# Kernel optimization log

Measured on AMD Instinct MI355X. Metric: run time of the kernel, lower is better.

## Reference

```python
import jax, jax.numpy as jnp
import numpy as np

B, N, H, S = 128, 20, 128, 2   # batch, num_nodes (= sequence_size), hidden, static feats
STEPS = 5 * N                  # max_steps in the torch loop; mask=depot=ones never breaks


def setup_inputs() -> dict:
    key = jax.random.key(0)
    ks = jax.random.split(key, 16)
    rn = lambda k, shape, s=0.1: jax.random.normal(k, shape, dtype=jnp.float32) * s
    z = lambda shape: jnp.zeros(shape, jnp.float32)
    return {
        "adj": jax.random.uniform(ks[0], (B, N, N), dtype=jnp.float32),
        "static": jax.random.uniform(ks[1], (B, S, N), dtype=jnp.float32),
        "dynamic": jax.random.uniform(ks[2], (B, S, N), dtype=jnp.float32),
        "depot": jnp.ones((B, N), jnp.float32),   # mask; log(1)=0 so never masks out
        # 1x1 Conv1d encoders == per-node linear maps (H, C_in)
        "W_adj": rn(ks[3], (H, N + 1)), "b_adj": z((H,)),
        "W_stat": rn(ks[4], (H, S)), "b_stat": z((H,)),
        "W_dyn": rn(ks[5], (H, S)), "b_dyn": z((H,)),
        "W_dec": rn(ks[6], (H, S)), "b_dec": z((H,)),
        # GRU (1 layer), torch gate order: r, z, n
        "gru_Wih": rn(ks[7], (3 * H, H)), "gru_Whh": rn(ks[8], (3 * H, H)),
        "gru_bih": z((3 * H,)), "gru_bhh": z((3 * H,)),
        # Attention: v (H,), W (H, 4H) over concat(adj_h, static_h, dyn_h, rnn)
        "attn_v": rn(ks[9], (H,)), "attn_W": rn(ks[10], (H, 4 * H)),
        # Pointer head: v (H,), W (H, 2H) over concat(static_h, context)
        "ptr_v": rn(ks[11], (H,)), "ptr_W": rn(ks[12], (H, 2 * H)),
        "x0": z((S,)),  # initial decoder input (torch: zeros)
    }


def reference(adj, static, dynamic, depot,
              W_adj, b_adj, W_stat, b_stat, W_dyn, b_dyn, W_dec, b_dec,
              gru_Wih, gru_Whh, gru_bih, gru_bhh,
              attn_v, attn_W, ptr_v, ptr_W, x0):
    # encode once (1x1 convs)
    adj_in = jnp.concatenate([adj, depot[:, None, :]], axis=1)      # (B, N+1, N)
    adj_h = jnp.einsum('hc,bcn->bhn', W_adj, adj_in) + b_adj[None, :, None]
    stat_h = jnp.einsum('hc,bcn->bhn', W_stat, static) + b_stat[None, :, None]
    dyn_h = jnp.einsum('hc,bcn->bhn', W_dyn, dynamic) + b_dyn[None, :, None]

    # split concat-weight into per-block matrices; precompute step-invariant parts
    Wa1, Wa2, Wa3, Wa4 = (attn_W[:, i * H:(i + 1) * H] for i in range(4))
    attn_pre = (jnp.einsum('hk,bkn->bhn', Wa1, adj_h)
                + jnp.einsum('hk,bkn->bhn', Wa2, stat_h)
                + jnp.einsum('hk,bkn->bhn', Wa3, dyn_h))            # (B, H, N)
    Wp1, Wp2 = ptr_W[:, :H], ptr_W[:, H:]
    ptr_pre = jnp.einsum('hk,bkn->bhn', Wp1, stat_h)                # (B, H, N)
    log_mask = jnp.log(depot)                                       # (B, N)

    def gru_cell(x, h):  # single-step GRU, torch semantics
        gi = x @ gru_Wih.T + gru_bih
        gh = h @ gru_Whh.T + gru_bhh
        r = jax.nn.sigmoid(gi[:, :H] + gh[:, :H])
        zg = jax.nn.sigmoid(gi[:, H:2 * H] + gh[:, H:2 * H])
        n = jnp.tanh(gi[:, 2 * H:] + r * gh[:, 2 * H:])
        return (1.0 - zg) * n + zg * h

    def step(carry, _):
        dec_in, h = carry
        dec_h = dec_in @ W_dec.T + b_dec                            # decoder 1x1 conv (B,H)
        h_new = gru_cell(dec_h, h)                                  # rnn_out == new hidden
        # tanh-attention over nodes: v . tanh(W @ concat(...))
        a = jnp.einsum('h,bhn->bn', attn_v,
                       jnp.tanh(attn_pre + (h_new @ Wa4.T)[:, :, None]))
        attn = jax.nn.softmax(a, axis=1)                            # (B, N)
        ctx = jnp.einsum('bn,bhn->bh', attn, stat_h)                # context (B, H)
        p = jnp.einsum('h,bhn->bn', ptr_v,
                       jnp.tanh(ptr_pre + (ctx @ Wp2.T)[:, :, None]))
        lsm = jax.nn.log_softmax(p + log_mask, axis=1)              # masked log-probs
        ptr = jnp.argmax(lsm, axis=1)                               # eval path: greedy
        logp = jnp.max(lsm, axis=1)                                 # log of max prob
        new_dec = jax.lax.stop_gradient(
            jnp.take_along_axis(static, ptr[:, None, None], axis=2)[:, :, 0])
        return (new_dec, h_new), (ptr, logp)

    dec0 = jnp.broadcast_to(x0[None, :], (B, S))
    h0 = jnp.zeros((B, H), static.dtype)
    _, (ptrs, logps) = jax.lax.scan(step, (dec0, h0), None, length=STEPS)
    tour_idx = ptrs.T        # (B, STEPS)
    tour_logp = logps.T      # (B, STEPS)
    return dynamic, tour_idx, tour_logp
```

## Files before the change

### kernel.cpp

```cpp
#include <hip/hip_runtime.h>
#include <math.h>

#define Bn 128
#define Nn 20
#define Hn 128
#define Sn 2
#define STEPS 100
#define NTHREADS 768

__device__ __forceinline__ float wredMaxAll(float v){
  #pragma unroll
  for (int o = 32; o; o >>= 1) v = fmaxf(v, __shfl_xor(v, o));
  return v;
}
__device__ __forceinline__ float wredSumAll(float v){
  #pragma unroll
  for (int o = 32; o; o >>= 1) v += __shfl_xor(v, o);
  return v;
}
__device__ __forceinline__ float frcp_(float x){ return __builtin_amdgcn_rcpf(x); }
__device__ __forceinline__ float ftanh(float x){
  float e = __expf(2.0f * x);
  return 1.0f - 2.0f * frcp_(e + 1.0f);
}
__device__ __forceinline__ float fsig(float x){ return frcp_(1.0f + __expf(-x)); }

__global__ __launch_bounds__(NTHREADS) void cvrp_ptr_net_kernel(
    const float* __restrict__ adj,   const float* __restrict__ stat,
    const float* __restrict__ dyn,   const float* __restrict__ depot,
    const float* __restrict__ W_adj, const float* __restrict__ b_adj,
    const float* __restrict__ W_stat,const float* __restrict__ b_stat,
    const float* __restrict__ W_dyn, const float* __restrict__ b_dyn,
    const float* __restrict__ W_dec, const float* __restrict__ b_dec,
    const float* __restrict__ Wih,   const float* __restrict__ Whh,
    const float* __restrict__ bih,   const float* __restrict__ bhh,
    const float* __restrict__ attn_v,const float* __restrict__ attn_W,
    const float* __restrict__ ptr_v, const float* __restrict__ ptr_W,
    const float* __restrict__ x0,
    float* __restrict__ out_idx, float* __restrict__ out_logp)
{
  __shared__ float s_attn_pre[Hn][Nn + 1];
  __shared__ float s_ptr_pre[Hn][Nn + 1];
  __shared__ float s_p2s[Hn][Nn + 1];
  __shared__ float s_eA[Hn][Nn + 1];
  __shared__ float s_eS[Hn][Nn + 1];
  __shared__ float s_eD[Hn][Nn + 1];
  __shared__ float s_adj[Nn][Nn];
  __shared__ float s_dep[Nn];
  __shared__ float s_st[Sn][Nn];
  __shared__ float s_dy[Sn][Nn];
  __shared__ float s_wdec0[Hn], s_wdec1[Hn], s_bdec[Hn];
  __shared__ float s_av[Hn], s_pv[Hn];
  __shared__ __align__(16) float s_h[Hn];
  __shared__ float s_a[2 * Hn];
  __shared__ float s_gin[Hn], s_ghn[Hn];
  __shared__ float s_q[Hn];
  __shared__ float s_sc[Nn];
  __shared__ float s_u[Hn];
  __shared__ float s_p[Nn];
  __shared__ float s_lm[Nn];

  const int b = blockIdx.x;
  const int t = threadIdx.x;
  const int wv = t >> 6;
  const int ln = t & 63;

  const int rrow  = wv * 32 + (ln & 31);
  const int rhalf = ln >> 5;
  const int qrow   = wv * 16 + (ln & 15);
  const int qquart = ln >> 4;

  for (int i = t; i < Nn * Nn; i += NTHREADS) s_adj[i / Nn][i % Nn] = adj[b * Nn * Nn + i];
  if (t < Nn) { float d = depot[b * Nn + t]; s_dep[t] = d; s_lm[t] = logf(d); }
  for (int i = t; i < Sn * Nn; i += NTHREADS) {
    s_st[i / Nn][i % Nn] = stat[b * Sn * Nn + i];
    s_dy[i / Nn][i % Nn] = dyn[b * Sn * Nn + i];
  }
  if (t < Hn) {
    s_wdec0[t] = W_dec[t * Sn]; s_wdec1[t] = W_dec[t * Sn + 1]; s_bdec[t] = b_dec[t];
    s_av[t] = attn_v[t]; s_pv[t] = ptr_v[t];
    s_h[t] = 0.0f;
  }
  __syncthreads();

  for (int idx = t; idx < Hn * Nn; idx += NTHREADS) {
    int h = idx / Nn, n = idx - h * Nn;
    const float* wa = W_adj + h * (Nn + 1);
    float accA = b_adj[h];
    #pragma unroll
    for (int c = 0; c < Nn; ++c) accA += wa[c] * s_adj[c][n];
    accA += wa[Nn] * s_dep[n];
    s_eA[h][n] = accA;
    s_eS[h][n] = b_stat[h] + W_stat[h * Sn] * s_st[0][n] + W_stat[h * Sn + 1] * s_st[1][n];
    s_eD[h][n] = b_dyn[h]  + W_dyn[h * Sn]  * s_dy[0][n] + W_dyn[h * Sn + 1]  * s_dy[1][n];
  }
  __syncthreads();

  for (int idx = t; idx < Hn * Nn; idx += NTHREADS) {
    int h = idx / Nn, n = idx - h * Nn;
    const float* aw = attn_W + h * (4 * Hn);
    const float* pw = ptr_W + h * (2 * Hn);
    float acc = 0.f, p1 = 0.f, p2 = 0.f;
    for (int k = 0; k < Hn; ++k) {
      float es = s_eS[k][n];
      acc += aw[k] * s_eA[k][n] + aw[Hn + k] * es + aw[2 * Hn + k] * s_eD[k][n];
      p1  += pw[k] * es;
      p2  += pw[Hn + k] * es;
    }
    s_attn_pre[h][n] = acc; s_ptr_pre[h][n] = p1; s_p2s[h][n] = p2;
  }

  float g0 = 0.f, g1 = 0.f, gc = 0.f;
  {
    const float* wi = Wih + rrow * Hn;
    for (int j = 0; j < Hn; ++j) {
      float w = wi[j];
      g0 += w * s_wdec0[j]; g1 += w * s_wdec1[j]; gc += w * s_bdec[j];
    }
    gc += bih[rrow];
  }
  const float bhh_r = bhh[rrow];

  float wrowh[64];
  {
    const float4* src = (const float4*)(Whh + rrow * Hn + rhalf * 64);
    #pragma unroll
    for (int c = 0; c < 16; ++c) {
      float4 v = src[c];
      wrowh[4 * c] = v.x; wrowh[4 * c + 1] = v.y; wrowh[4 * c + 2] = v.z; wrowh[4 * c + 3] = v.w;
    }
  }
  float wa4q[32];
  if (t < 512) {
    const float4* src = (const float4*)(attn_W + qrow * 4 * Hn + 3 * Hn + qquart * 32);
    #pragma unroll
    for (int c = 0; c < 8; ++c) {
      float4 v = src[c];
      wa4q[4 * c] = v.x; wa4q[4 * c + 1] = v.y; wa4q[4 * c + 2] = v.z; wa4q[4 * c + 3] = v.w;
    }
  }
  __syncthreads();

  float dec0 = x0[0], dec1 = x0[1];
  float gh_reg = bhh_r;
  float* oi = out_idx + b * STEPS;
  float* ol = out_logp + b * STEPS;

  for (int step = 0; step < STEPS; ++step) {
    if ((ln >> 5) == 0) {
      float gi = g0 * dec0 + g1 * dec1 + gc;
      if (rrow < 2 * Hn) s_a[rrow] = gi + gh_reg;
      else { s_gin[rrow - 2 * Hn] = gi; s_ghn[rrow - 2 * Hn] = gh_reg; }
    }
    __syncthreads();

    if (t < Hn) {
      float rr = fsig(s_a[t]);
      float zz = fsig(s_a[Hn + t]);
      float nn = ftanh(s_gin[t] + rr * s_ghn[t]);
      s_h[t] = (1.0f - zz) * nn + zz * s_h[t];
    }
    __syncthreads();

    {
      if (t < 512) {
        float qp = 0.f;
        const float4* hh = (const float4*)(s_h + qquart * 32);
        #pragma unroll
        for (int c = 0; c < 8; ++c) {
          float4 hv = hh[c];
          qp += wa4q[4 * c] * hv.x + wa4q[4 * c + 1] * hv.y
              + wa4q[4 * c + 2] * hv.z + wa4q[4 * c + 3] * hv.w;
        }
        qp += __shfl_xor(qp, 16);
        qp += __shfl_xor(qp, 32);
        if (ln < 16) s_q[qrow] = qp;
      }
      float a0 = 0.f, a1 = 0.f, a2 = 0.f, a3 = 0.f;
      const float4* h4 = (const float4*)(s_h + rhalf * 64);
      #pragma unroll
      for (int c = 0; c < 16; ++c) {
        float4 hv = h4[c];
        a0 += wrowh[4 * c] * hv.x; a1 += wrowh[4 * c + 1] * hv.y;
        a2 += wrowh[4 * c + 2] * hv.z; a3 += wrowh[4 * c + 3] * hv.w;
      }
      float part = (a0 + a1) + (a2 + a3);
      part += __shfl_xor(part, 32);
      gh_reg = bhh_r + part;
    }
    __syncthreads();

    if (t < 32 * Nn) {
      int n = t >> 5, g = t & 31;
      float part = 0.f;
      #pragma unroll
      for (int i = 0; i < 4; ++i) {
        int h2 = g * 4 + ((i + g) & 3);
        part += s_av[h2] * ftanh(s_attn_pre[h2][n] + s_q[h2]);
      }
      part += __shfl_xor(part, 16);
      part += __shfl_xor(part, 8);
      part += __shfl_xor(part, 4);
      part += __shfl_xor(part, 2);
      part += __shfl_xor(part, 1);
      if (g == 0) s_sc[n] = part;
    }
    __syncthreads();

    if (t < Hn) {
      int lane = t & 63;
      float v = (lane < Nn) ? s_sc[lane] : -INFINITY;
      float m = wredMaxAll(v);
      float e = (lane < Nn) ? __expf(v - m) : 0.f;
      float ssum = wredSumAll(e);
      float inv = frcp_(ssum);
      float acc = 0.f;
      #pragma unroll
      for (int n = 0; n < Nn; ++n) {
        float an = __shfl(e, n);
        acc += s_p2s[t][n] * an;
      }
      s_u[t] = acc * inv;
    }
    __syncthreads();

    if (t < 32 * Nn) {
      int n = t >> 5, g = t & 31;
      float part = 0.f;
      #pragma unroll
      for (int i = 0; i < 4; ++i) {
        int h2 = g * 4 + ((i + g) & 3);
        part += s_pv[h2] * ftanh(s_ptr_pre[h2][n] + s_u[h2]);
      }
      part += __shfl_xor(part, 16);
      part += __shfl_xor(part, 8);
      part += __shfl_xor(part, 4);
      part += __shfl_xor(part, 2);
      part += __shfl_xor(part, 1);
      if (g == 0) s_p[n] = part;
    }
    __syncthreads();

    {
      float v = (ln < Nn) ? (s_p[ln] + s_lm[ln]) : -INFINITY;
      float m = wredMaxAll(v);
      unsigned long long mask = __ballot(v == m);
      int amax = __ffsll(mask) - 1;
      dec0 = s_st[0][amax];
      dec1 = s_st[1][amax];
      if (t < 64) {
        float e = (ln < Nn) ? __expf(v - m) : 0.f;
        float ssum = wredSumAll(e);
        if (t == 0) {
          oi[step] = (float)amax;
          ol[step] = -__logf(ssum);
        }
      }
    }
  }
}

extern "C" void kernel_launch(void* const* d_in, const int* in_sizes, int n_in,
                              void* d_out, int out_size, void* d_ws, size_t ws_size,
                              hipStream_t stream) {
  (void)in_sizes; (void)n_in; (void)d_ws; (void)ws_size; (void)out_size;
  const float* adj    = (const float*)d_in[0];
  const float* stat   = (const float*)d_in[1];
  const float* dynp   = (const float*)d_in[2];
  const float* depot  = (const float*)d_in[3];
  const float* W_adj  = (const float*)d_in[4];
  const float* b_adj  = (const float*)d_in[5];
  const float* W_stat = (const float*)d_in[6];
  const float* b_stat = (const float*)d_in[7];
  const float* W_dyn  = (const float*)d_in[8];
  const float* b_dyn  = (const float*)d_in[9];
  const float* W_dec  = (const float*)d_in[10];
  const float* b_dec  = (const float*)d_in[11];
  const float* Wih    = (const float*)d_in[12];
  const float* Whh    = (const float*)d_in[13];
  const float* bih    = (const float*)d_in[14];
  const float* bhh    = (const float*)d_in[15];
  const float* attn_v = (const float*)d_in[16];
  const float* attn_W = (const float*)d_in[17];
  const float* ptr_v  = (const float*)d_in[18];
  const float* ptr_W  = (const float*)d_in[19];
  const float* x0     = (const float*)d_in[20];

  float* out = (float*)d_out;
  hipMemcpyAsync(out, dynp, (size_t)Bn * Sn * Nn * sizeof(float),
                 hipMemcpyDeviceToDevice, stream);
  float* out_idx  = out + Bn * Sn * Nn;
  float* out_logp = out + Bn * Sn * Nn + Bn * STEPS;

  cvrp_ptr_net_kernel<<<Bn, NTHREADS, 0, stream>>>(
      adj, stat, dynp, depot, W_adj, b_adj, W_stat, b_stat, W_dyn, b_dyn,
      W_dec, b_dec, Wih, Whh, bih, bhh, attn_v, attn_W, ptr_v, ptr_W, x0,
      out_idx, out_logp);
}
```

Measured before the change: 544.1 us.

## Fold GRU input gates into update threads and drop per-step barrier

Threads 0..127 now hold all three input-gate coefficient sets and compute gi_r/gi_z/gi_n directly. The hidden-gate matvec results go to a shared s_gh buffer, initialised with bhh, instead of being staged through s_a/s_gin/s_ghn. This removes one __syncthreads and one shared-memory staging phase from each of the 100 sequential steps. It also changes the attention and pointer h-index mapping to a strided i*32+g pattern and splits the softmax-weighted context accumulation into four independent chains to shorten the dependency chain.

```diff
diff --git a/kernel.cpp b/kernel.cpp
--- a/kernel.cpp
+++ b/kernel.cpp
@@ -52,8 +52,7 @@
   __shared__ float s_wdec0[Hn], s_wdec1[Hn], s_bdec[Hn];
   __shared__ float s_av[Hn], s_pv[Hn];
   __shared__ __align__(16) float s_h[Hn];
-  __shared__ float s_a[2 * Hn];
-  __shared__ float s_gin[Hn], s_ghn[Hn];
+  __shared__ float s_gh[3 * Hn];
   __shared__ float s_q[Hn];
   __shared__ float s_sc[Nn];
   __shared__ float s_u[Hn];
@@ -81,6 +80,7 @@
     s_av[t] = attn_v[t]; s_pv[t] = ptr_v[t];
     s_h[t] = 0.0f;
   }
+  if (t < 3 * Hn) s_gh[t] = bhh[t];
   __syncthreads();
 
   for (int idx = t; idx < Hn * Nn; idx += NTHREADS) {
@@ -110,14 +110,21 @@
     s_attn_pre[h][n] = acc; s_ptr_pre[h][n] = p1; s_p2s[h][n] = p2;
   }
 
-  float g0 = 0.f, g1 = 0.f, gc = 0.f;
-  {
-    const float* wi = Wih + rrow * Hn;
+  float c_r0 = 0.f, c_r1 = 0.f, c_rc = 0.f;
+  float c_z0 = 0.f, c_z1 = 0.f, c_zc = 0.f;
+  float c_n0 = 0.f, c_n1 = 0.f, c_nc = 0.f;
+  if (t < Hn) {
+    const float* wr_ = Wih + t * Hn;
+    const float* wz_ = Wih + (Hn + t) * Hn;
+    const float* wn_ = Wih + (2 * Hn + t) * Hn;
     for (int j = 0; j < Hn; ++j) {
-      float w = wi[j];
-      g0 += w * s_wdec0[j]; g1 += w * s_wdec1[j]; gc += w * s_bdec[j];
-    }
-    gc += bih[rrow];
+      float d0 = s_wdec0[j], d1 = s_wdec1[j], db = s_bdec[j];
+      float wr = wr_[j], wz = wz_[j], wn = wn_[j];
+      c_r0 += wr * d0; c_r1 += wr * d1; c_rc += wr * db;
+      c_z0 += wz * d0; c_z1 += wz * d1; c_zc += wz * db;
+      c_n0 += wn * d0; c_n1 += wn * d1; c_nc += wn * db;
+    }
+    c_rc += bih[t]; c_zc += bih[Hn + t]; c_nc += bih[2 * Hn + t];
   }
   const float bhh_r = bhh[rrow];
 
@@ -142,22 +149,18 @@
   __syncthreads();
 
   float dec0 = x0[0], dec1 = x0[1];
-  float gh_reg = bhh_r;
   float* oi = out_idx + b * STEPS;
   float* ol = out_logp + b * STEPS;
 
   for (int step = 0; step < STEPS; ++step) {
-    if ((ln >> 5) == 0) {
-      float gi = g0 * dec0 + g1 * dec1 + gc;
-      if (rrow < 2 * Hn) s_a[rrow] = gi + gh_reg;
-      else { s_gin[rrow - 2 * Hn] = gi; s_ghn[rrow - 2 * Hn] = gh_reg; }
-    }
-    __syncthreads();
-
     if (t < Hn) {
-      float rr = fsig(s_a[t]);
-      float zz = fsig(s_a[Hn + t]);
-      float nn = ftanh(s_gin[t] + rr * s_ghn[t]);
+      float gh_r = s_gh[t], gh_z = s_gh[Hn + t], gh_n = s_gh[2 * Hn + t];
+      float gi_r = c_r0 * dec0 + c_r1 * dec1 + c_rc;
+      float gi_z = c_z0 * dec0 + c_z1 * dec1 + c_zc;
+      float gi_n = c_n0 * dec0 + c_n1 * dec1 + c_nc;
+      float rr = fsig(gi_r + gh_r);
+      float zz = fsig(gi_z + gh_z);
+      float nn = ftanh(gi_n + rr * gh_n);
       s_h[t] = (1.0f - zz) * nn + zz * s_h[t];
     }
     __syncthreads();
@@ -186,7 +189,7 @@
       }
       float part = (a0 + a1) + (a2 + a3);
       part += __shfl_xor(part, 32);
-      gh_reg = bhh_r + part;
+      if ((ln >> 5) == 0) s_gh[rrow] = bhh_r + part;
     }
     __syncthreads();
 
@@ -195,7 +198,7 @@
       float part = 0.f;
       #pragma unroll
       for (int i = 0; i < 4; ++i) {
-        int h2 = g * 4 + ((i + g) & 3);
+        int h2 = i * 32 + g;
         part += s_av[h2] * ftanh(s_attn_pre[h2][n] + s_q[h2]);
       }
       part += __shfl_xor(part, 16);
@@ -214,13 +217,15 @@
       float e = (lane < Nn) ? __expf(v - m) : 0.f;
       float ssum = wredSumAll(e);
       float inv = frcp_(ssum);
-      float acc = 0.f;
+      float a0 = 0.f, a1 = 0.f, a2 = 0.f, a3 = 0.f;
       #pragma unroll
-      for (int n = 0; n < Nn; ++n) {
-        float an = __shfl(e, n);
-        acc += s_p2s[t][n] * an;
-      }
-      s_u[t] = acc * inv;
+      for (int n = 0; n < Nn; n += 4) {
+        a0 += s_p2s[t][n]     * __shfl(e, n);
+        a1 += s_p2s[t][n + 1] * __shfl(e, n + 1);
+        a2 += s_p2s[t][n + 2] * __shfl(e, n + 2);
+        a3 += s_p2s[t][n + 3] * __shfl(e, n + 3);
+      }
+      s_u[t] = ((a0 + a1) + (a2 + a3)) * inv;
     }
     __syncthreads();
 
@@ -229,7 +234,7 @@
       float part = 0.f;
       #pragma unroll
       for (int i = 0; i < 4; ++i) {
-        int h2 = g * 4 + ((i + g) & 3);
+        int h2 = i * 32 + g;
         part += s_pv[h2] * ftanh(s_ptr_pre[h2][n] + s_u[h2]);
       }
       part += __shfl_xor(part, 16);
```

Result: faster. 465.9 us (-14.4%).
